# Kernel tuning notes

Hardware: AMD Instinct MI355X
Metric: run time of the kernel (lower is better)

## Reference

```python
import jax, jax.numpy as jnp
import numpy as np

P, F, FR = 288, 7, 12      # time slots per day, days per week, sampling frequency scale
CHEB_K = 2
HID = 64


def _ste(time_index, SE, W_se, b_se, T_tod, T_dow):
    """Spatio-temporal embedding: learned spatial embedding projected to et_dim,
    plus time-of-day and day-of-week temporal embeddings. -> [B, N, et]"""
    t = time_index * FR
    tod = T_tod[t % P]                 # [B, et]
    dow = T_dow[(t // P) % F]          # [B, et]
    se = SE @ W_se + b_se              # [N, et]
    return se[None, :, :] + (tod + dow)[:, None, :]


def _avwgcn(x, STE, R, SC, Wpool, bpool):
    """Adaptive-vertex-weight graph conv (AGCRN-style) with dynamic STE-driven
    adjacency blended with dynamic relation R and static correlation SC.
    x: [B,N,Cin], STE: [B,N,et], R: [B,N,N], SC: [N,N]."""
    A = jax.nn.softmax(
        jax.nn.relu(jnp.einsum('bnd,bmd->bnm', STE, STE)) + R + SC[None], axis=-1)
    # Chebyshev polynomial supports applied to x (T0 = I handled implicitly)
    xs = [x, jnp.einsum('bnm,bmc->bnc', A, x)]
    for _ in range(CHEB_K - 2):
        xs.append(2.0 * jnp.einsum('bnm,bmc->bnc', A, xs[-1]) - xs[-2])
    x_g = jnp.stack(xs, axis=2)                        # [B,N,K,Cin]
    # per-node adaptive weights: W_n = STE @ Wpool; contracted without
    # materializing the [B,N,K,Cin,Cout] tensor
    g = jnp.einsum('bnki,dkio->bndo', x_g, Wpool)      # [B,N,et,Cout]
    out = jnp.einsum('bndo,bnd->bno', g, STE) + jnp.einsum('bnd,do->bno', STE, bpool)
    return out


def setup_inputs() -> dict:
    key = jax.random.key(0)
    ks = jax.random.split(key, 12)
    B, N, Din, et, es = 32, 1024, 1, 16, 16
    std = 0.1
    return {
        "x": jax.random.normal(ks[0], (B, N, Din), jnp.float32),
        "R": jax.random.normal(ks[1], (B, N, N), jnp.float32) * std,
        "state": jax.random.normal(ks[2], (B, N, HID), jnp.float32),
        "SC": jax.random.normal(ks[3], (N, N), jnp.float32) * std,
        "SE": jax.random.normal(ks[4], (N, es), jnp.float32),
        "W_se": jax.random.normal(ks[5], (es, et), jnp.float32) * std,
        "b_se": jnp.zeros((et,), jnp.float32),
        "T_tod": jax.random.normal(ks[6], (P, et), jnp.float32) * std,
        "T_dow": jax.random.normal(ks[7], (F, et), jnp.float32) * std,
        "W_gate": jax.random.normal(ks[8], (et, CHEB_K, Din + HID, 2 * HID), jnp.float32) * std,
        "b_gate": jnp.zeros((et, 2 * HID), jnp.float32),
        "W_upd": jax.random.normal(ks[9], (et, CHEB_K, Din + HID, HID), jnp.float32) * std,
        "b_upd": jnp.zeros((et, HID), jnp.float32),
        "time_index": jax.random.randint(ks[10], (B,), 0, P * F),
    }


def reference(x, R, state, SC, SE, W_se, b_se, T_tod, T_dow,
              W_gate, b_gate, W_upd, b_upd, time_index):
    STE = _ste(time_index, SE, W_se, b_se, T_tod, T_dow)       # [B,N,et]
    ins = jnp.concatenate([x, state], axis=-1)                 # [B,N,Din+H]
    z_r = jax.nn.sigmoid(_avwgcn(ins, STE, R, SC, W_gate, b_gate))
    z, r = jnp.split(z_r, 2, axis=-1)                          # each [B,N,H]
    cand = jnp.concatenate([x, z * state], axis=-1)
    hc = jnp.tanh(_avwgcn(cand, STE, R, SC, W_upd, b_upd))
    return r * state + (1.0 - r) * hc                          # [B,N,H]
```

## Files before the change

kernel.cpp:

```cpp
#include <hip/hip_runtime.h>
#include <math.h>

namespace {
constexpr int BB = 32;
constexpr int NN = 1024;
constexpr int ET = 16;
constexpr int HH = 64;
constexpr int CIN = 65;
constexpr int KI = 2*CIN;
constexpr int COG = 2*HH;
constexpr int COU = HH;
constexpr int PP = 288;
constexpr int FF = 7;
constexpr int FRQ = 12;
constexpr int XK = 160;

typedef __attribute__((ext_vector_type(4))) float f32x4;
typedef __attribute__((ext_vector_type(8))) short s16x8;
typedef unsigned long long ull;

__device__ __forceinline__ float bf2f(unsigned short u) {
    unsigned v = ((unsigned)u) << 16;
    return __builtin_bit_cast(float, v);
}
__device__ __forceinline__ unsigned short f2bf(float f) {
    unsigned u = __builtin_bit_cast(unsigned, f);
    u += 0x7fffu + ((u >> 16) & 1u);
    return (unsigned short)(u >> 16);
}
__device__ __forceinline__ unsigned cvtpk(float lo, float hi) {
    unsigned r;
    asm("v_cvt_pk_bf16_f32 %0, %1, %2" : "=v"(r) : "v"(lo), "v"(hi));
    return r;
}
__device__ __forceinline__ float ldany(const float* p) { return *p; }
__device__ __forceinline__ float ldany(const unsigned short* p) { return bf2f(*p); }

__global__ void k_prep1(const float* __restrict__ SE, const float* __restrict__ Wse,
                        const float* __restrict__ bse, const float* __restrict__ Ttod,
                        const float* __restrict__ Tdow, const int* __restrict__ tidx,
                        float* __restrict__ se, float* __restrict__ tt) {
    int idx = blockIdx.x*blockDim.x + threadIdx.x;
    if (idx < NN*ET) {
        int n = idx / ET, d = idx % ET;
        float acc = bse[d];
        #pragma unroll
        for (int e = 0; e < ET; ++e) acc += SE[n*ET + e]*Wse[e*ET + d];
        se[idx] = acc;
    } else if (idx < NN*ET + BB*ET) {
        int r = idx - NN*ET;
        int b = r / ET, d = r % ET;
        int t = tidx[b]*FRQ;
        tt[r] = Ttod[(t % PP)*ET + d] + Tdow[((t/PP) % FF)*ET + d];
    }
}

__global__ void k_prep2(const float* __restrict__ se, const float* __restrict__ tt,
                        const float* __restrict__ Wg, const float* __restrict__ Wu,
                        unsigned short* __restrict__ stebf,
                        unsigned short* __restrict__ Wptg, unsigned short* __restrict__ Wptu) {
    int idx = blockIdx.x*blockDim.x + threadIdx.x;
    if (idx < BB*NN*ET) {
        int d = idx % ET;
        int n = (idx/ET) % NN;
        int b = idx/(ET*NN);
        stebf[idx] = f2bf(se[n*ET+d] + tt[b*ET+d]);
        return;
    }
    idx -= BB*NN*ET;
    if (idx < ET*COG*XK) {
        int d = idx/(COG*XK), r = idx%(COG*XK), o = r/XK, ki = r%XK;
        float v = (ki < KI) ? Wg[((size_t)d*KI + ki)*COG + o] : 0.f;
        Wptg[((size_t)d*COG + o)*XK + ki] = f2bf(v);
        return;
    }
    idx -= ET*COG*XK;
    if (idx < ET*COU*XK) {
        int d = idx/(COU*XK), r = idx%(COU*XK), o = r/XK, ki = r%XK;
        float v = (ki < KI) ? Wu[((size_t)d*KI + ki)*COU + o] : 0.f;
        Wptu[((size_t)d*COU + o)*XK + ki] = f2bf(v);
    }
}

template<typename T>
__global__ void k_vin(const float* __restrict__ x, const T* __restrict__ sv,
                      unsigned short* __restrict__ xgbf, unsigned short* __restrict__ vt) {
    int idx = blockIdx.x*blockDim.x + threadIdx.x;
    if (idx < BB*128*64) {
        int och = idx & 63, mb = (idx >> 6) & 127, b = idx >> 13;
        const T* src = sv + ((size_t)b*NN + mb*8)*HH + och;
        float v0=ldany(src), v1=ldany(src+HH), v2=ldany(src+2*HH), v3=ldany(src+3*HH);
        float v4=ldany(src+4*HH), v5=ldany(src+5*HH), v6=ldany(src+6*HH), v7=ldany(src+7*HH);
        ull lo = (ull)f2bf(v0) | ((ull)f2bf(v1)<<16) | ((ull)f2bf(v2)<<32) | ((ull)f2bf(v3)<<48);
        ull hi = (ull)f2bf(v4) | ((ull)f2bf(v5)<<16) | ((ull)f2bf(v6)<<32) | ((ull)f2bf(v7)<<48);
        ull* dst = (ull*)(vt + (size_t)idx*8);
        dst[0] = lo; dst[1] = hi;
        return;
    }
    idx -= BB*128*64;
    if (idx >= BB*NN*(XK/2)) return;
    int row = idx/(XK/2), c = idx%(XK/2);
    if (c < 32) {
        int k0 = 2*c;
        float v0 = (k0 == 0) ? x[row] : ldany(sv + (size_t)row*HH + k0 - 1);
        float v1 = ldany(sv + (size_t)row*HH + k0);
        ((unsigned*)xgbf)[(size_t)row*(XK/2) + c] = ((unsigned)f2bf(v1) << 16) | f2bf(v0);
    } else if (c == 32) {
        xgbf[(size_t)row*XK + 64] = f2bf(ldany(sv + (size_t)row*HH + 63));
    } else if (c >= 65) {
        ((unsigned*)xgbf)[(size_t)row*(XK/2) + c] = 0;
    }
}

constexpr int SSTR   = 1048;
constexpr int S_OFF  = 0;
constexpr int XV_OFF = 33536;
constexpr int MSH_OFF  = 37632;
constexpr int MSHC_OFF = 37888;
constexpr int LP_OFF   = 37952;
constexpr int AXP_OFF  = 38208;
constexpr int LSH_OFF  = 38464;
constexpr int SMEM_BYTES = 38528;

template<int PASS>
__global__ __launch_bounds__(256, 4) void k_attn(
    const unsigned short* __restrict__ stebf, const float* __restrict__ Rg,
    const float* __restrict__ SCg, const float* __restrict__ xg,
    const unsigned short* __restrict__ vt,
    float* __restrict__ Mr, float* __restrict__ Li,
    unsigned short* __restrict__ xgout)
{
    extern __shared__ char smem[];
    const int t = threadIdx.x, lane = t & 63, w = t >> 6;
    const int c15 = lane & 15, g = lane >> 4;
    const int strip = blockIdx.x, b = blockIdx.y;
    const size_t bN = (size_t)b * NN;
    const int r0 = strip * 16;

    float* Mshf  = (float*)(smem + MSH_OFF);
    float* MshCf = (float*)(smem + MSHC_OFF);
    float* Lpf   = (float*)(smem + LP_OFF);
    float* Axpf  = (float*)(smem + AXP_OFF);
    float* Lshf  = (float*)(smem + LSH_OFF);

    if (PASS == 1) {
        ((float4*)(smem + XV_OFF))[t] = ((const float4*)(xg + bN))[t];
    } else {
        if (t < 16) Lshf[t] = Li[bN + r0 + t];
    }
    float mp2 = 0.f;
    if (PASS == 2) mp2 = Mr[bN + r0 + c15];

    float mx = -INFINITY;
    {
        s16x8 bfr = {0,0,0,0,0,0,0,0};
        if (g < 2) bfr = *(const s16x8*)(stebf + (bN + r0 + c15)*ET + g*8);
        const float* Rb  = Rg  + (bN + r0 + c15)*NN;
        const float* SCb = SCg + (size_t)(r0 + c15)*NN;
        const int colq = w*16 + g*4;
        float4 rc = *(const float4*)(Rb + colq);
        float4 sc = *(const float4*)(SCb + colq);
        for (int j = 0; j < 16; ++j) {
            s16x8 af = {0,0,0,0,0,0,0,0};
            if (g < 2) af = *(const s16x8*)(stebf + (bN + j*64 + w*16 + c15)*ET + g*8);
            float4 rn = {0,0,0,0}, sn = {0,0,0,0};
            if (j < 15) {
                rn = *(const float4*)(Rb + colq + (j+1)*64);
                sn = *(const float4*)(SCb + colq + (j+1)*64);
            }
            f32x4 zero = {0.f,0.f,0.f,0.f};
            f32x4 d = __builtin_amdgcn_mfma_f32_16x16x32_bf16(af, bfr, zero, 0, 0, 0);
            float s0 = fmaxf(d[0],0.f) + rc.x + sc.x;
            float s1 = fmaxf(d[1],0.f) + rc.y + sc.y;
            float s2 = fmaxf(d[2],0.f) + rc.z + sc.z;
            float s3 = fmaxf(d[3],0.f) + rc.w + sc.w;
            unsigned byteo = (unsigned)(c15*SSTR + j*64 + colq)*2u;
            if (PASS == 1) {
                mx = fmaxf(mx, fmaxf(fmaxf(s0,s1), fmaxf(s2,s3)));
                *(ull*)(smem + S_OFF + byteo) = (ull)cvtpk(s0,s1) | ((ull)cvtpk(s2,s3) << 32);
            } else {
                float p0 = __expf(s0 - mp2), p1 = __expf(s1 - mp2);
                float p2 = __expf(s2 - mp2), p3 = __expf(s3 - mp2);
                *(ull*)(smem + S_OFF + byteo) = (ull)cvtpk(p0,p1) | ((ull)cvtpk(p2,p3) << 32);
            }
            rc = rn; sc = sn;
        }
    }

    if (PASS == 1) {
        mx = fmaxf(mx, __shfl_xor(mx, 16));
        mx = fmaxf(mx, __shfl_xor(mx, 32));
        if (lane < 16) Mshf[w*16 + c15] = mx;
        __syncthreads();
        if (t < 16) {
            float M = fmaxf(fmaxf(Mshf[t], Mshf[16+t]), fmaxf(Mshf[32+t], Mshf[48+t]));
            MshCf[t] = M;
            Mr[bN + r0 + t] = M;
        }
        __syncthreads();
        const float m = MshCf[c15];
        const int colq = w*16 + g*4;
        float L = 0.f, ax = 0.f;
        for (int it = 0; it < 16; ++it) {
            unsigned byteo = (unsigned)(c15*SSTR + it*64 + colq)*2u;
            ull v = *(ull*)(smem + S_OFF + byteo);
            float s0 = bf2f((unsigned short)v);
            float s1 = bf2f((unsigned short)(v >> 16));
            float s2 = bf2f((unsigned short)(v >> 32));
            float s3 = bf2f((unsigned short)(v >> 48));
            float p0 = __expf(s0-m), p1 = __expf(s1-m), p2 = __expf(s2-m), p3 = __expf(s3-m);
            float4 xq = *(const float4*)(smem + XV_OFF + (it*64 + colq)*4);
            L += (p0 + p1) + (p2 + p3);
            ax += p0*xq.x + p1*xq.y + p2*xq.z + p3*xq.w;
            *(ull*)(smem + S_OFF + byteo) = (ull)cvtpk(p0,p1) | ((ull)cvtpk(p2,p3) << 32);
        }
        L += __shfl_xor(L, 16); L += __shfl_xor(L, 32);
        ax += __shfl_xor(ax, 16); ax += __shfl_xor(ax, 32);
        if (lane < 16) { Lpf[w*16 + c15] = L; Axpf[w*16 + c15] = ax; }
        __syncthreads();
        if (t < 16) {
            float Lt = Lpf[t] + Lpf[16+t] + Lpf[32+t] + Lpf[48+t];
            float li = 1.f / Lt;
            Lshf[t] = li;
            Li[bN + r0 + t] = li;
            float axt = Axpf[t] + Axpf[16+t] + Axpf[32+t] + Axpf[48+t];
            xgout[(bN + r0 + t)*XK + 65] = f2bf(axt * li);
        }
        __syncthreads();
    } else {
        __syncthreads();
    }

    {
        f32x4 acc = {0.f,0.f,0.f,0.f};
        const unsigned short* vtb = vt + ((size_t)b*128*64 + (w*16 + c15))*8;
        #pragma unroll 4
        for (int j = 0; j < 16; ++j) {
            #pragma unroll
            for (int ks = 0; ks < 2; ++ks) {
                s16x8 a  = *(const s16x8*)(smem + S_OFF + (unsigned)(c15*SSTR + j*64 + ks*32 + g*8)*2u);
                s16x8 bv = *(const s16x8*)(vtb + (size_t)(j*8 + ks*4 + g)*512);
                acc = __builtin_amdgcn_mfma_f32_16x16x32_bf16(a, bv, acc, 0, 0, 0);
            }
        }
        #pragma unroll
        for (int q = 0; q < 4; ++q) {
            int rowl = g*4 + q;
            float li = Lshf[rowl];
            xgout[(bN + r0 + rowl)*XK + 66 + w*16 + c15] = f2bf(acc[q] * li);
        }
    }
}

template<int COUT, int EPI>
__global__ __launch_bounds__(256, 2) void k_apply(
    const unsigned short* __restrict__ Wpt, const float* __restrict__ bias,
    const unsigned short* __restrict__ stebf, const unsigned short* __restrict__ xgbf,
    const float* __restrict__ state, unsigned short* __restrict__ zsbf,
    unsigned short* __restrict__ rrbf, float* __restrict__ out)
{
    const int t = threadIdx.x, lane = t & 63, w = t >> 6;
    const int c15 = lane & 15, g = lane >> 4;
    const int n0 = blockIdx.x*32, b = blockIdx.y, oh = blockIdx.z;
    const int o = oh*64 + w*16 + c15;

    f32x4 acc[16][2];
    #pragma unroll
    for (int d = 0; d < 16; ++d) {
        acc[d][0] = (f32x4){0.f,0.f,0.f,0.f};
        acc[d][1] = (f32x4){0.f,0.f,0.f,0.f};
    }

    const unsigned short* Ar0 = xgbf + ((size_t)b*NN + n0 + c15)*XK + g*8;
    const unsigned short* Ar1 = Ar0 + (size_t)16*XK;
    const unsigned short* Bp  = Wpt + (size_t)o*XK + g*8;

    for (int ks = 0; ks < 5; ++ks) {
        s16x8 a0 = *(const s16x8*)(Ar0 + ks*32);
        s16x8 a1 = *(const s16x8*)(Ar1 + ks*32);
        #pragma unroll
        for (int d = 0; d < 16; ++d) {
            s16x8 bf = *(const s16x8*)(Bp + (size_t)d*COUT*XK + ks*32);
            acc[d][0] = __builtin_amdgcn_mfma_f32_16x16x32_bf16(a0, bf, acc[d][0], 0, 0, 0);
            acc[d][1] = __builtin_amdgcn_mfma_f32_16x16x32_bf16(a1, bf, acc[d][1], 0, 0, 0);
        }
    }

    float biasv[16];
    #pragma unroll
    for (int d = 0; d < 16; ++d) biasv[d] = bias[d*COUT + o];

    #pragma unroll
    for (int mt = 0; mt < 2; ++mt) {
        #pragma unroll
        for (int q = 0; q < 4; ++q) {
            int n = n0 + mt*16 + g*4 + q;
            size_t bn = (size_t)b*NN + n;
            const ull* sp = (const ull*)(stebf + bn*ET);
            float val = 0.f;
            #pragma unroll
            for (int dd = 0; dd < 4; ++dd) {
                ull sv4 = sp[dd];
                float s0 = bf2f((unsigned short)sv4);
                float s1 = bf2f((unsigned short)(sv4 >> 16));
                float s2 = bf2f((unsigned short)(sv4 >> 32));
                float s3 = bf2f((unsigned short)(sv4 >> 48));
                val += s0*(acc[dd*4+0][mt][q] + biasv[dd*4+0]);
                val += s1*(acc[dd*4+1][mt][q] + biasv[dd*4+1]);
                val += s2*(acc[dd*4+2][mt][q] + biasv[dd*4+2]);
                val += s3*(acc[dd*4+3][mt][q] + biasv[dd*4+3]);
            }
            if (EPI == 0) {
                float gv = 1.f/(1.f + __expf(-val));
                if (oh == 0) zsbf[bn*HH + o] = f2bf(gv * state[bn*HH + o]);
                else         rrbf[bn*HH + (o - 64)] = f2bf(gv);
            } else {
                float hc = tanhf(val);
                float rv = bf2f(rrbf[bn*HH + o]);
                out[bn*HH + o] = rv*state[bn*HH + o] + (1.f - rv)*hc;
            }
        }
    }
}

}

extern "C" void kernel_launch(void* const* d_in, const int* in_sizes, int n_in,
                              void* d_out, int out_size, void* d_ws, size_t ws_size,
                              hipStream_t stream) {
    const float* x     = (const float*)d_in[0];
    const float* R     = (const float*)d_in[1];
    const float* state = (const float*)d_in[2];
    const float* SC    = (const float*)d_in[3];
    const float* SE    = (const float*)d_in[4];
    const float* W_se  = (const float*)d_in[5];
    const float* b_se  = (const float*)d_in[6];
    const float* T_tod = (const float*)d_in[7];
    const float* T_dow = (const float*)d_in[8];
    const float* W_g   = (const float*)d_in[9];
    const float* b_g   = (const float*)d_in[10];
    const float* W_u   = (const float*)d_in[11];
    const float* b_u   = (const float*)d_in[12];
    const int*   tidx  = (const int*)d_in[13];
    float* out = (float*)d_out;
    float* ws = (float*)d_ws;

    float* se = ws;
    float* tt = se + 16384;
    float* Mr = tt + 512;
    float* Li = Mr + 32768;
    unsigned short* stebf = (unsigned short*)(Li + 32768);
    unsigned short* xgbf  = stebf + 524288;
    unsigned short* zsbf  = xgbf + 5242880;
    unsigned short* rrbf  = zsbf + 2097152;
    unsigned short* vt    = rrbf + 2097152;
    unsigned short* Wptg  = vt + 2097152;
    unsigned short* Wptu  = Wptg + 327680;

    k_prep1<<<66, 256, 0, stream>>>(SE, W_se, b_se, T_tod, T_dow, tidx, se, tt);
    k_prep2<<<3968, 256, 0, stream>>>(se, tt, W_g, W_u, stebf, Wptg, Wptu);

    k_vin<float><<<11264, 256, 0, stream>>>(x, state, xgbf, vt);
    k_attn<1><<<dim3(64, 32), 256, SMEM_BYTES, stream>>>(
        stebf, R, SC, x, vt, Mr, Li, xgbf);
    k_apply<COG, 0><<<dim3(32, 32, 2), 256, 0, stream>>>(
        Wptg, b_g, stebf, xgbf, state, zsbf, rrbf, nullptr);

    k_vin<unsigned short><<<11264, 256, 0, stream>>>(x, zsbf, xgbf, vt);
    k_attn<2><<<dim3(64, 32), 256, SMEM_BYTES, stream>>>(
        stebf, R, SC, x, vt, Mr, Li, xgbf);
    k_apply<COU, 1><<<dim3(32, 32, 1), 256, 0, stream>>>(
        Wptu, b_u, stebf, xgbf, state, zsbf, rrbf, out);
}
```

Before: 233.6 us.

## Cache softmax probabilities in global memory and skip recomputation in second pass

The first attention pass now also writes the bf16 softmax probabilities to a global buffer when the workspace is large enough. The second pass then runs a new P·V-only kernel instead of reloading R and SC and recomputing the scores and exponentials. This replaces about 256 MB of fp32 R/SC reads with a 64 MB bf16 write plus a 64 MB read. The change also software-pipelines the R/SC/STE loads and the V loads two iterations ahead in k_attn. It depends on the workspace size, so it is unclear whether the cached path runs by default.

```diff
diff --git a/kernel.cpp b/kernel.cpp
--- a/kernel.cpp
+++ b/kernel.cpp
@@ -128,7 +128,7 @@
     const float* __restrict__ SCg, const float* __restrict__ xg,
     const unsigned short* __restrict__ vt,
     float* __restrict__ Mr, float* __restrict__ Li,
-    unsigned short* __restrict__ xgout)
+    unsigned short* __restrict__ xgout, unsigned short* __restrict__ pglob)
 {
     extern __shared__ char smem[];
     const int t = threadIdx.x, lane = t & 63, w = t >> 6;
@@ -158,22 +158,31 @@
         const float* Rb  = Rg  + (bN + r0 + c15)*NN;
         const float* SCb = SCg + (size_t)(r0 + c15)*NN;
         const int colq = w*16 + g*4;
-        float4 rc = *(const float4*)(Rb + colq);
-        float4 sc = *(const float4*)(SCb + colq);
+        s16x8 af0 = {0,0,0,0,0,0,0,0}, af1 = {0,0,0,0,0,0,0,0};
+        if (g < 2) {
+            af0 = *(const s16x8*)(stebf + (bN + 0*64 + w*16 + c15)*ET + g*8);
+            af1 = *(const s16x8*)(stebf + (bN + 1*64 + w*16 + c15)*ET + g*8);
+        }
+        float4 rc0 = *(const float4*)(Rb + colq);
+        float4 sc0 = *(const float4*)(SCb + colq);
+        float4 rc1 = *(const float4*)(Rb + colq + 64);
+        float4 sc1 = *(const float4*)(SCb + colq + 64);
+        #pragma unroll
         for (int j = 0; j < 16; ++j) {
-            s16x8 af = {0,0,0,0,0,0,0,0};
-            if (g < 2) af = *(const s16x8*)(stebf + (bN + j*64 + w*16 + c15)*ET + g*8);
-            float4 rn = {0,0,0,0}, sn = {0,0,0,0};
-            if (j < 15) {
-                rn = *(const float4*)(Rb + colq + (j+1)*64);
-                sn = *(const float4*)(SCb + colq + (j+1)*64);
+            s16x8 afc = af0; af0 = af1;
+            float4 rcc = rc0, scc = sc0;
+            rc0 = rc1; sc0 = sc1;
+            if (j < 14) {
+                if (g < 2) af1 = *(const s16x8*)(stebf + (bN + (j+2)*64 + w*16 + c15)*ET + g*8);
+                rc1 = *(const float4*)(Rb + colq + (j+2)*64);
+                sc1 = *(const float4*)(SCb + colq + (j+2)*64);
             }
             f32x4 zero = {0.f,0.f,0.f,0.f};
-            f32x4 d = __builtin_amdgcn_mfma_f32_16x16x32_bf16(af, bfr, zero, 0, 0, 0);
-            float s0 = fmaxf(d[0],0.f) + rc.x + sc.x;
-            float s1 = fmaxf(d[1],0.f) + rc.y + sc.y;
-            float s2 = fmaxf(d[2],0.f) + rc.z + sc.z;
-            float s3 = fmaxf(d[3],0.f) + rc.w + sc.w;
+            f32x4 d = __builtin_amdgcn_mfma_f32_16x16x32_bf16(afc, bfr, zero, 0, 0, 0);
+            float s0 = fmaxf(d[0],0.f) + rcc.x + scc.x;
+            float s1 = fmaxf(d[1],0.f) + rcc.y + scc.y;
+            float s2 = fmaxf(d[2],0.f) + rcc.z + scc.z;
+            float s3 = fmaxf(d[3],0.f) + rcc.w + scc.w;
             unsigned byteo = (unsigned)(c15*SSTR + j*64 + colq)*2u;
             if (PASS == 1) {
                 mx = fmaxf(mx, fmaxf(fmaxf(s0,s1), fmaxf(s2,s3)));
@@ -183,7 +192,6 @@
                 float p2 = __expf(s2 - mp2), p3 = __expf(s3 - mp2);
                 *(ull*)(smem + S_OFF + byteo) = (ull)cvtpk(p0,p1) | ((ull)cvtpk(p2,p3) << 32);
             }
-            rc = rn; sc = sn;
         }
     }
 
@@ -212,7 +220,9 @@
             float4 xq = *(const float4*)(smem + XV_OFF + (it*64 + colq)*4);
             L += (p0 + p1) + (p2 + p3);
             ax += p0*xq.x + p1*xq.y + p2*xq.z + p3*xq.w;
-            *(ull*)(smem + S_OFF + byteo) = (ull)cvtpk(p0,p1) | ((ull)cvtpk(p2,p3) << 32);
+            ull pk = (ull)cvtpk(p0,p1) | ((ull)cvtpk(p2,p3) << 32);
+            *(ull*)(smem + S_OFF + byteo) = pk;
+            if (pglob) *(ull*)(pglob + (bN + r0 + c15)*1024 + it*64 + colq) = pk;
         }
         L += __shfl_xor(L, 16); L += __shfl_xor(L, 32);
         ax += __shfl_xor(ax, 16); ax += __shfl_xor(ax, 32);
@@ -233,15 +243,15 @@
 
     {
         f32x4 acc = {0.f,0.f,0.f,0.f};
-        const unsigned short* vtb = vt + ((size_t)b*128*64 + (w*16 + c15))*8;
-        #pragma unroll 4
-        for (int j = 0; j < 16; ++j) {
-            #pragma unroll
-            for (int ks = 0; ks < 2; ++ks) {
-                s16x8 a  = *(const s16x8*)(smem + S_OFF + (unsigned)(c15*SSTR + j*64 + ks*32 + g*8)*2u);
-                s16x8 bv = *(const s16x8*)(vtb + (size_t)(j*8 + ks*4 + g)*512);
-                acc = __builtin_amdgcn_mfma_f32_16x16x32_bf16(a, bv, acc, 0, 0, 0);
-            }
+        const unsigned short* vtb = vt + (size_t)b*65536 + (w*16 + c15)*8 + g*512;
+        s16x8 bv0 = *(const s16x8*)(vtb);
+        s16x8 bv1 = *(const s16x8*)(vtb + 2048);
+        #pragma unroll
+        for (int kk = 0; kk < 32; ++kk) {
+            s16x8 bvc = bv0; bv0 = bv1;
+            if (kk < 30) bv1 = *(const s16x8*)(vtb + (size_t)(kk+2)*2048);
+            s16x8 a = *(const s16x8*)(smem + S_OFF + (unsigned)(c15*SSTR + kk*32 + g*8)*2u);
+            acc = __builtin_amdgcn_mfma_f32_16x16x32_bf16(a, bvc, acc, 0, 0, 0);
         }
         #pragma unroll
         for (int q = 0; q < 4; ++q) {
@@ -249,6 +259,49 @@
             float li = Lshf[rowl];
             xgout[(bN + r0 + rowl)*XK + 66 + w*16 + c15] = f2bf(acc[q] * li);
         }
+    }
+}
+
+__global__ __launch_bounds__(256) void k_pv2(
+    const unsigned short* __restrict__ pglob, const unsigned short* __restrict__ vt,
+    const float* __restrict__ Li, unsigned short* __restrict__ xgout)
+{
+    const int t = threadIdx.x, lane = t & 63, w = t >> 6;
+    const int c15 = lane & 15, g = lane >> 4;
+    const int b = blockIdx.y;
+    const int strip = blockIdx.x*4 + w;
+    const size_t bN = (size_t)b*NN;
+    const int r0 = strip*16;
+
+    const unsigned short* Pr  = pglob + (bN + r0 + c15)*1024 + g*8;
+    const unsigned short* vb0 = vt + (size_t)b*65536 + c15*8 + g*512;
+
+    f32x4 acc0 = {0,0,0,0}, acc1 = {0,0,0,0}, acc2 = {0,0,0,0}, acc3 = {0,0,0,0};
+    s16x8 a0 = *(const s16x8*)(Pr);
+    s16x8 a1 = *(const s16x8*)(Pr + 32);
+    #pragma unroll 8
+    for (int kk = 0; kk < 32; ++kk) {
+        s16x8 ac = a0; a0 = a1;
+        if (kk < 30) a1 = *(const s16x8*)(Pr + (kk+2)*32);
+        const unsigned short* vb = vb0 + (size_t)kk*2048;
+        s16x8 b0 = *(const s16x8*)(vb);
+        s16x8 b1 = *(const s16x8*)(vb + 128);
+        s16x8 b2 = *(const s16x8*)(vb + 256);
+        s16x8 b3 = *(const s16x8*)(vb + 384);
+        acc0 = __builtin_amdgcn_mfma_f32_16x16x32_bf16(ac, b0, acc0, 0, 0, 0);
+        acc1 = __builtin_amdgcn_mfma_f32_16x16x32_bf16(ac, b1, acc1, 0, 0, 0);
+        acc2 = __builtin_amdgcn_mfma_f32_16x16x32_bf16(ac, b2, acc2, 0, 0, 0);
+        acc3 = __builtin_amdgcn_mfma_f32_16x16x32_bf16(ac, b3, acc3, 0, 0, 0);
+    }
+    #pragma unroll
+    for (int q = 0; q < 4; ++q) {
+        int row = r0 + g*4 + q;
+        float li = Li[bN + row];
+        unsigned short* op = xgout + (bN + row)*XK + 66 + c15;
+        op[0]  = f2bf(acc0[q]*li);
+        op[16] = f2bf(acc1[q]*li);
+        op[32] = f2bf(acc2[q]*li);
+        op[48] = f2bf(acc3[q]*li);
     }
 }
 
@@ -356,19 +409,26 @@
     unsigned short* vt    = rrbf + 2097152;
     unsigned short* Wptg  = vt + 2097152;
     unsigned short* Wptu  = Wptg + 327680;
+    unsigned short* pglob = Wptu + 163840;
+    size_t need_bytes = (size_t)((char*)(pglob + 33554432) - (char*)ws);
+    const bool haveP = ws_size >= need_bytes;
 
     k_prep1<<<66, 256, 0, stream>>>(SE, W_se, b_se, T_tod, T_dow, tidx, se, tt);
     k_prep2<<<3968, 256, 0, stream>>>(se, tt, W_g, W_u, stebf, Wptg, Wptu);
 
     k_vin<float><<<11264, 256, 0, stream>>>(x, state, xgbf, vt);
     k_attn<1><<<dim3(64, 32), 256, SMEM_BYTES, stream>>>(
-        stebf, R, SC, x, vt, Mr, Li, xgbf);
+        stebf, R, SC, x, vt, Mr, Li, xgbf, haveP ? pglob : nullptr);
     k_apply<COG, 0><<<dim3(32, 32, 2), 256, 0, stream>>>(
         Wptg, b_g, stebf, xgbf, state, zsbf, rrbf, nullptr);
 
     k_vin<unsigned short><<<11264, 256, 0, stream>>>(x, zsbf, xgbf, vt);
-    k_attn<2><<<dim3(64, 32), 256, SMEM_BYTES, stream>>>(
-        stebf, R, SC, x, vt, Mr, Li, xgbf);
+    if (haveP) {
+        k_pv2<<<dim3(16, 32), 256, 0, stream>>>(pglob, vt, Li, xgbf);
+    } else {
+        k_attn<2><<<dim3(64, 32), 256, SMEM_BYTES, stream>>>(
+            stebf, R, SC, x, vt, Mr, Li, xgbf, nullptr);
+    }
     k_apply<COU, 1><<<dim3(32, 32, 1), 256, 0, stream>>>(
         Wptu, b_u, stebf, xgbf, state, zsbf, rrbf, out);
 }
```

Result: slower. 256.1 us (+9.6%).
